# Kernel tuning notes

Hardware: AMD Instinct MI355X
Metric: run time of the kernel (lower is better)

Reference implementation:

```python
import jax, jax.numpy as jnp
import numpy as np

H, W, D = 160, 160, 16
VOXEL_SIZE = 0.4
VOL_MIN = np.array([-32.0, -32.0, -1.0], dtype=np.float32)
SCALE_MULTIPLIER = 3.0
N_GAUSS = 8192
CHUNK = 64


def setup_inputs() -> dict:
    key = jax.random.key(0)
    k1, k2, k3, k4, k5 = jax.random.split(key, 5)
    vol_min = jnp.asarray(VOL_MIN)
    vol_ext = jnp.array([64.0, 64.0, 6.4], dtype=jnp.float32)
    means3d = jax.random.uniform(k1, (N_GAUSS, 3), jnp.float32) * vol_ext + vol_min
    opacities = jax.random.uniform(k2, (N_GAUSS, 1), jnp.float32)
    # per-axis std devs: 0.2..0.8 m so 3-sigma footprint spans a handful of voxels
    scales = 0.2 + 0.6 * jax.random.uniform(k3, (N_GAUSS, 3), jnp.float32)
    rotations = jax.random.normal(k4, (N_GAUSS, 4), jnp.float32)
    features = jax.random.normal(k5, (N_GAUSS, 32), jnp.float32)
    return {"means3d": means3d, "opacities": opacities, "scales": scales,
            "rotations": rotations, "features": features}


def quat_to_rotmat(q):
    # q: [N,4] wxyz, normalized
    w, x, y, z = q[:, 0], q[:, 1], q[:, 2], q[:, 3]
    R = jnp.stack([
        jnp.stack([1 - 2 * (y * y + z * z), 2 * (x * y - w * z), 2 * (x * z + w * y)], -1),
        jnp.stack([2 * (x * y + w * z), 1 - 2 * (x * x + z * z), 2 * (y * z - w * x)], -1),
        jnp.stack([2 * (x * z - w * y), 2 * (y * z + w * x), 1 - 2 * (x * x + y * y)], -1),
    ], axis=-2)  # [N,3,3]
    return R


def _grid_coords():
    ii, jj, kk = jnp.meshgrid(jnp.arange(H), jnp.arange(W), jnp.arange(D), indexing="ij")
    idx = jnp.stack([ii, jj, kk], axis=-1).astype(jnp.float32)
    return (idx + 0.5) * VOXEL_SIZE + jnp.asarray(VOL_MIN)  # [H,W,D,3] voxel centers


def reference(means3d, opacities, scales, rotations, features):
    x = _grid_coords().reshape(-1, 3)  # [V,3]
    q = rotations / jnp.linalg.norm(rotations, axis=-1, keepdims=True)
    R = quat_to_rotmat(q)
    # covariance = R diag(s^2) R^T
    cov = jnp.einsum("nij,nj,nkj->nik", R, scales * scales, R)
    cov_inv = jnp.linalg.inv(cov)
    sigma = jnp.sqrt(jnp.diagonal(cov, axis1=1, axis2=2))  # [N,3]
    opac = opacities[:, 0]  # [N]
    n = means3d.shape[0]
    nchunks = n // CHUNK

    def chunked(a):
        return a.reshape(nchunks, CHUNK, *a.shape[1:])

    def step(acc, c):
        mu, op, sg, ci, ft = c
        diff = x[:, None, :] - mu[None, :, :]  # [V,CHUNK,3]
        maha = jnp.einsum("vci,cij,vcj->vc", diff, ci, diff)
        # local aggregation cutoff: within scale_multiplier * sigma box around mean
        mask = jnp.all(jnp.abs(diff) <= SCALE_MULTIPLIER * sg[None, :, :], axis=-1)
        w = op[None, :] * jnp.exp(-0.5 * maha) * mask  # [V,CHUNK]
        return acc + w @ ft, None

    acc0 = jnp.zeros((x.shape[0], features.shape[-1]), jnp.float32)
    xs = (chunked(means3d), chunked(opac), chunked(sigma), chunked(cov_inv), chunked(features))
    acc, _ = jax.lax.scan(step, acc0, xs)
    return acc.reshape(H, W, D, features.shape[-1])
```

## Files before the change

### kernel.cpp

```cpp
#include <hip/hip_runtime.h>

#define HH 160
#define WW 160
#define DD 16
#define NG 8192
#define VOXEL 0.4f

#define TTX 20
#define TTY 20
#define TTZ 4
#define NTILES (TTX * TTY * TTZ)
#define CAP 128


__global__ __launch_bounds__(64) void gv_precompute_bin(
    const float* __restrict__ means, const float* __restrict__ opac,
    const float* __restrict__ scales, const float* __restrict__ rots,
    int* __restrict__ tileCnt, float4* __restrict__ tilePack) {
  int g = blockIdx.x * 64 + threadIdx.x;
  if (g >= NG) return;
  float qw = rots[g * 4 + 0], qx = rots[g * 4 + 1];
  float qy = rots[g * 4 + 2], qz = rots[g * 4 + 3];
  float inv = rsqrtf(qw * qw + qx * qx + qy * qy + qz * qz);
  qw *= inv; qx *= inv; qy *= inv; qz *= inv;
  float R[3][3];
  R[0][0] = 1.f - 2.f * (qy * qy + qz * qz);
  R[0][1] = 2.f * (qx * qy - qw * qz);
  R[0][2] = 2.f * (qx * qz + qw * qy);
  R[1][0] = 2.f * (qx * qy + qw * qz);
  R[1][1] = 1.f - 2.f * (qx * qx + qz * qz);
  R[1][2] = 2.f * (qy * qz - qw * qx);
  R[2][0] = 2.f * (qx * qz - qw * qy);
  R[2][1] = 2.f * (qy * qz + qw * qx);
  R[2][2] = 1.f - 2.f * (qx * qx + qy * qy);
  float sx = scales[g * 3 + 0], sy = scales[g * 3 + 1], sz = scales[g * 3 + 2];
  float s2[3] = {sx * sx, sy * sy, sz * sz};
  float is2[3] = {1.f / s2[0], 1.f / s2[1], 1.f / s2[2]};
  float cov00 = 0.f, cov11 = 0.f, cov22 = 0.f;
  float ci00 = 0.f, ci01 = 0.f, ci02 = 0.f, ci11 = 0.f, ci12 = 0.f, ci22 = 0.f;
#pragma unroll
  for (int c = 0; c < 3; c++) {
    cov00 += R[0][c] * R[0][c] * s2[c];
    cov11 += R[1][c] * R[1][c] * s2[c];
    cov22 += R[2][c] * R[2][c] * s2[c];
    ci00 += R[0][c] * R[0][c] * is2[c];
    ci01 += R[0][c] * R[1][c] * is2[c];
    ci02 += R[0][c] * R[2][c] * is2[c];
    ci11 += R[1][c] * R[1][c] * is2[c];
    ci12 += R[1][c] * R[2][c] * is2[c];
    ci22 += R[2][c] * R[2][c] * is2[c];
  }
  float mx = means[g * 3 + 0], my = means[g * 3 + 1], mz = means[g * 3 + 2];
  float bx = 3.f * sqrtf(cov00), by = 3.f * sqrtf(cov11), bz = 3.f * sqrtf(cov22);

  const float eps = 1e-4f;
  int i0 = (int)ceilf((mx - bx + 32.f) * 2.5f - 0.5f - eps);
  int i1 = (int)floorf((mx + bx + 32.f) * 2.5f - 0.5f + eps);
  int j0 = (int)ceilf((my - by + 32.f) * 2.5f - 0.5f - eps);
  int j1 = (int)floorf((my + by + 32.f) * 2.5f - 0.5f + eps);
  int k0 = (int)ceilf((mz - bz + 1.f) * 2.5f - 0.5f - eps);
  int k1 = (int)floorf((mz + bz + 1.f) * 2.5f - 0.5f + eps);
  i0 = max(i0, 0); i1 = min(i1, HH - 1);
  j0 = max(j0, 0); j1 = min(j1, WW - 1);
  k0 = max(k0, 0); k1 = min(k1, DD - 1);
  if (i0 > i1 || j0 > j1 || k0 > k1) return;

  float4 p0 = make_float4(mx, my, mz, opac[g]);
  float4 p1 = make_float4(bx, by, bz, __int_as_float(g));
  float4 p2 = make_float4(ci00, ci01, ci02, ci11);
  float4 p3 = make_float4(ci12, ci22, 0.f, 0.f);

  int ti0 = i0 >> 3, ti1 = i1 >> 3;
  int tj0 = j0 >> 3, tj1 = j1 >> 3;
  int tk0 = k0 >> 2, tk1 = k1 >> 2;
  for (int ti = ti0; ti <= ti1; ti++)
    for (int tj = tj0; tj <= tj1; tj++)
      for (int tk = tk0; tk <= tk1; tk++) {
        int t = (ti * TTY + tj) * TTZ + tk;
        int pos = atomicAdd(&tileCnt[t], 1);
        if (pos < CAP) {
          float4* __restrict__ d = tilePack + ((size_t)t * CAP + pos) * 4;
          d[0] = p0;  d[1] = p1;  d[2] = p2;  d[3] = p3;
        }
      }
}

__global__ __launch_bounds__(256) void gv_voxelize(
    const float4* __restrict__ feats, const int* __restrict__ tileCnt,
    const float4* __restrict__ tilePack, float4* __restrict__ out) {
  __shared__ float4 s_pack[CAP * 4];

  int tid = threadIdx.x;
  int dk = tid & 3, dj = (tid >> 2) & 7, di = tid >> 5;
  int tk = blockIdx.x, tj = blockIdx.y, ti = blockIdx.z;
  int i = ti * 8 + di, j = tj * 8 + dj, k = tk * 4 + dk;

  float px = (i + 0.5f) * VOXEL - 32.f;
  float py = (j + 0.5f) * VOXEL - 32.f;
  float pz = (k + 0.5f) * VOXEL - 1.f;

  int t = (ti * TTY + tj) * TTZ + tk;
  int cnt = tileCnt[t];
  cnt = min(cnt, CAP);

  {
    const float4* __restrict__ src = tilePack + (size_t)t * CAP * 4;
    int tot = cnt * 4;
    for (int m = tid; m < tot; m += 256) s_pack[m] = src[m];
  }
  __syncthreads();

  float4 acc[8];
#pragma unroll
  for (int f = 0; f < 8; f++) acc[f] = make_float4(0.f, 0.f, 0.f, 0.f);

  int n = 0;
  for (; n + 2 <= cnt; n += 2) {
    float4 a0 = s_pack[n * 4 + 0], b0 = s_pack[n * 4 + 1];
    float4 a1 = s_pack[n * 4 + 4], b1 = s_pack[n * 4 + 5];

    int g0 = __builtin_amdgcn_readfirstlane(__float_as_int(b0.w));
    int g1 = __builtin_amdgcn_readfirstlane(__float_as_int(b1.w));
    const float4* __restrict__ fp0 = feats + (size_t)g0 * 8;
    const float4* __restrict__ fp1 = feats + (size_t)g1 * 8;
    float4 F0[8], F1[8];
#pragma unroll
    for (int f = 0; f < 8; f++) F0[f] = fp0[f];
#pragma unroll
    for (int f = 0; f < 8; f++) F1[f] = fp1[f];

    float dx0 = px - a0.x, dy0 = py - a0.y, dz0 = pz - a0.z;
    float dx1 = px - a1.x, dy1 = py - a1.y, dz1 = pz - a1.z;
    bool in0 = (fabsf(dx0) <= b0.x) & (fabsf(dy0) <= b0.y) & (fabsf(dz0) <= b0.z);
    bool in1 = (fabsf(dx1) <= b1.x) & (fabsf(dy1) <= b1.y) & (fabsf(dz1) <= b1.z);

    if (__any(in0)) {
      float4 c0 = s_pack[n * 4 + 2], d0 = s_pack[n * 4 + 3];
      float maha = c0.x * dx0 * dx0 + c0.w * dy0 * dy0 + d0.y * dz0 * dz0 +
                   2.f * (c0.y * dx0 * dy0 + c0.z * dx0 * dz0 + d0.x * dy0 * dz0);
      float wgt = in0 ? a0.w * __expf(-0.5f * maha) : 0.f;
#pragma unroll
      for (int f = 0; f < 8; f++) {
        acc[f].x += wgt * F0[f].x;
        acc[f].y += wgt * F0[f].y;
        acc[f].z += wgt * F0[f].z;
        acc[f].w += wgt * F0[f].w;
      }
    }
    if (__any(in1)) {
      float4 c1 = s_pack[n * 4 + 6], d1 = s_pack[n * 4 + 7];
      float maha = c1.x * dx1 * dx1 + c1.w * dy1 * dy1 + d1.y * dz1 * dz1 +
                   2.f * (c1.y * dx1 * dy1 + c1.z * dx1 * dz1 + d1.x * dy1 * dz1);
      float wgt = in1 ? a1.w * __expf(-0.5f * maha) : 0.f;
#pragma unroll
      for (int f = 0; f < 8; f++) {
        acc[f].x += wgt * F1[f].x;
        acc[f].y += wgt * F1[f].y;
        acc[f].z += wgt * F1[f].z;
        acc[f].w += wgt * F1[f].w;
      }
    }
  }
  if (n < cnt) {
    float4 pa = s_pack[n * 4 + 0], pb = s_pack[n * 4 + 1];
    int gg = __builtin_amdgcn_readfirstlane(__float_as_int(pb.w));
    const float4* __restrict__ fp = feats + (size_t)gg * 8;
    float dx = px - pa.x, dy = py - pa.y, dz = pz - pa.z;
    bool in = (fabsf(dx) <= pb.x) & (fabsf(dy) <= pb.y) & (fabsf(dz) <= pb.z);
    if (__any(in)) {
      float4 pc = s_pack[n * 4 + 2], pd = s_pack[n * 4 + 3];
      float maha = pc.x * dx * dx + pc.w * dy * dy + pd.y * dz * dz +
                   2.f * (pc.y * dx * dy + pc.z * dx * dz + pd.x * dy * dz);
      float wgt = in ? pa.w * __expf(-0.5f * maha) : 0.f;
#pragma unroll
      for (int f = 0; f < 8; f++) {
        float4 fv = fp[f];
        acc[f].x += wgt * fv.x;
        acc[f].y += wgt * fv.y;
        acc[f].z += wgt * fv.z;
        acc[f].w += wgt * fv.w;
      }
    }
  }

  size_t v = ((size_t)i * WW + j) * DD + k;
  float4* o = out + v * 8;
#pragma unroll
  for (int f = 0; f < 8; f++) o[f] = acc[f];
}

extern "C" void kernel_launch(void* const* d_in, const int* in_sizes, int n_in,
                              void* d_out, int out_size, void* d_ws, size_t ws_size,
                              hipStream_t stream) {
  const float* means  = (const float*)d_in[0];
  const float* opac   = (const float*)d_in[1];
  const float* scales = (const float*)d_in[2];
  const float* rots   = (const float*)d_in[3];
  const float4* feats = (const float4*)d_in[4];

  char* ws = (char*)d_ws;
  int* tileCnt     = (int*)ws;
  float4* tilePack = (float4*)(ws + 64 * 1024);

  hipMemsetAsync(tileCnt, 0, NTILES * sizeof(int), stream);
  gv_precompute_bin<<<128, 64, 0, stream>>>(means, opac, scales, rots,
                                            tileCnt, tilePack);
  dim3 grid(TTZ, TTY, TTX);
  gv_voxelize<<<grid, 256, 0, stream>>>(feats, tileCnt, tilePack,
                                        (float4*)d_out);
}
```

Measured before the change: 121.9 us.

## Compute two voxels per thread to reuse gaussian loads and shared terms

Each thread now handles two voxels at j and j+4, so the block shrinks to 128 threads and every lane reuses one set of loaded gaussian features and shared mahalanobis terms (x/z parts) across both voxels. This cuts the per-voxel cost of feature loads, LDS reads, wave-level any-votes and loop overhead. The trade-off is twice the accumulator registers, which may lower occupancy, and fewer waves per block. The any-vote now covers a union of two voxel rows, so some waves may run gaussians that only one of their voxels needs.

```diff
diff --git a/kernel.cpp b/kernel.cpp
--- a/kernel.cpp
+++ b/kernel.cpp
@@ -85,18 +85,20 @@
       }
 }
 
-__global__ __launch_bounds__(256) void gv_voxelize(
+__global__ __launch_bounds__(128) void gv_voxelize(
     const float4* __restrict__ feats, const int* __restrict__ tileCnt,
     const float4* __restrict__ tilePack, float4* __restrict__ out) {
   __shared__ float4 s_pack[CAP * 4];
 
   int tid = threadIdx.x;
-  int dk = tid & 3, dj = (tid >> 2) & 7, di = tid >> 5;
+  int wid = tid >> 6, l = tid & 63;
+  int dk = l & 3, dj = (l >> 2) & 3, di = wid * 4 + (l >> 4);
   int tk = blockIdx.x, tj = blockIdx.y, ti = blockIdx.z;
-  int i = ti * 8 + di, j = tj * 8 + dj, k = tk * 4 + dk;
+  int i = ti * 8 + di, jA = tj * 8 + dj, jB = jA + 4, k = tk * 4 + dk;
 
   float px = (i + 0.5f) * VOXEL - 32.f;
-  float py = (j + 0.5f) * VOXEL - 32.f;
+  float pyA = (jA + 0.5f) * VOXEL - 32.f;
+  float pyB = (jB + 0.5f) * VOXEL - 32.f;
   float pz = (k + 0.5f) * VOXEL - 1.f;
 
   int t = (ti * TTY + tj) * TTZ + tk;
@@ -106,13 +108,41 @@
   {
     const float4* __restrict__ src = tilePack + (size_t)t * CAP * 4;
     int tot = cnt * 4;
-    for (int m = tid; m < tot; m += 256) s_pack[m] = src[m];
+    for (int m = tid; m < tot; m += 128) s_pack[m] = src[m];
   }
   __syncthreads();
 
-  float4 acc[8];
-#pragma unroll
-  for (int f = 0; f < 8; f++) acc[f] = make_float4(0.f, 0.f, 0.f, 0.f);
+  float4 accA[8], accB[8];
+#pragma unroll
+  for (int f = 0; f < 8; f++) {
+    accA[f] = make_float4(0.f, 0.f, 0.f, 0.f);
+    accB[f] = make_float4(0.f, 0.f, 0.f, 0.f);
+  }
+
+#define GAUSS_BODY(aa, bb, cidx, didx, FF)                                    \
+  do {                                                                        \
+    float dx = px - aa.x, dz = pz - aa.z;                                     \
+    float dyA = pyA - aa.y, dyB = pyB - aa.y;                                 \
+    bool okx = (fabsf(dx) <= bb.x) & (fabsf(dz) <= bb.z);                     \
+    bool inA = okx & (fabsf(dyA) <= bb.y);                                    \
+    bool inB = okx & (fabsf(dyB) <= bb.y);                                    \
+    if (__any(inA | inB)) {                                                   \
+      float4 cc = s_pack[cidx], dd = s_pack[didx];                            \
+      float base = cc.x * dx * dx + dd.y * dz * dz + 2.f * cc.z * dx * dz;    \
+      float u = 2.f * (cc.y * dx + dd.x * dz);                                \
+      float mA = base + dyA * (cc.w * dyA + u);                               \
+      float mB = base + dyB * (cc.w * dyB + u);                               \
+      float wA = inA ? aa.w * __expf(-0.5f * mA) : 0.f;                       \
+      float wB = inB ? aa.w * __expf(-0.5f * mB) : 0.f;                       \
+      _Pragma("unroll")                                                       \
+      for (int f = 0; f < 8; f++) {                                           \
+        accA[f].x += wA * FF[f].x; accA[f].y += wA * FF[f].y;                 \
+        accA[f].z += wA * FF[f].z; accA[f].w += wA * FF[f].w;                 \
+        accB[f].x += wB * FF[f].x; accB[f].y += wB * FF[f].y;                 \
+        accB[f].z += wB * FF[f].z; accB[f].w += wB * FF[f].w;                 \
+      }                                                                       \
+    }                                                                         \
+  } while (0)
 
   int n = 0;
   for (; n + 2 <= cnt; n += 2) {
@@ -129,64 +159,28 @@
 #pragma unroll
     for (int f = 0; f < 8; f++) F1[f] = fp1[f];
 
-    float dx0 = px - a0.x, dy0 = py - a0.y, dz0 = pz - a0.z;
-    float dx1 = px - a1.x, dy1 = py - a1.y, dz1 = pz - a1.z;
-    bool in0 = (fabsf(dx0) <= b0.x) & (fabsf(dy0) <= b0.y) & (fabsf(dz0) <= b0.z);
-    bool in1 = (fabsf(dx1) <= b1.x) & (fabsf(dy1) <= b1.y) & (fabsf(dz1) <= b1.z);
-
-    if (__any(in0)) {
-      float4 c0 = s_pack[n * 4 + 2], d0 = s_pack[n * 4 + 3];
-      float maha = c0.x * dx0 * dx0 + c0.w * dy0 * dy0 + d0.y * dz0 * dz0 +
-                   2.f * (c0.y * dx0 * dy0 + c0.z * dx0 * dz0 + d0.x * dy0 * dz0);
-      float wgt = in0 ? a0.w * __expf(-0.5f * maha) : 0.f;
-#pragma unroll
-      for (int f = 0; f < 8; f++) {
-        acc[f].x += wgt * F0[f].x;
-        acc[f].y += wgt * F0[f].y;
-        acc[f].z += wgt * F0[f].z;
-        acc[f].w += wgt * F0[f].w;
-      }
-    }
-    if (__any(in1)) {
-      float4 c1 = s_pack[n * 4 + 6], d1 = s_pack[n * 4 + 7];
-      float maha = c1.x * dx1 * dx1 + c1.w * dy1 * dy1 + d1.y * dz1 * dz1 +
-                   2.f * (c1.y * dx1 * dy1 + c1.z * dx1 * dz1 + d1.x * dy1 * dz1);
-      float wgt = in1 ? a1.w * __expf(-0.5f * maha) : 0.f;
-#pragma unroll
-      for (int f = 0; f < 8; f++) {
-        acc[f].x += wgt * F1[f].x;
-        acc[f].y += wgt * F1[f].y;
-        acc[f].z += wgt * F1[f].z;
-        acc[f].w += wgt * F1[f].w;
-      }
-    }
+    GAUSS_BODY(a0, b0, n * 4 + 2, n * 4 + 3, F0);
+    GAUSS_BODY(a1, b1, n * 4 + 6, n * 4 + 7, F1);
   }
   if (n < cnt) {
     float4 pa = s_pack[n * 4 + 0], pb = s_pack[n * 4 + 1];
     int gg = __builtin_amdgcn_readfirstlane(__float_as_int(pb.w));
     const float4* __restrict__ fp = feats + (size_t)gg * 8;
-    float dx = px - pa.x, dy = py - pa.y, dz = pz - pa.z;
-    bool in = (fabsf(dx) <= pb.x) & (fabsf(dy) <= pb.y) & (fabsf(dz) <= pb.z);
-    if (__any(in)) {
-      float4 pc = s_pack[n * 4 + 2], pd = s_pack[n * 4 + 3];
-      float maha = pc.x * dx * dx + pc.w * dy * dy + pd.y * dz * dz +
-                   2.f * (pc.y * dx * dy + pc.z * dx * dz + pd.x * dy * dz);
-      float wgt = in ? pa.w * __expf(-0.5f * maha) : 0.f;
-#pragma unroll
-      for (int f = 0; f < 8; f++) {
-        float4 fv = fp[f];
-        acc[f].x += wgt * fv.x;
-        acc[f].y += wgt * fv.y;
-        acc[f].z += wgt * fv.z;
-        acc[f].w += wgt * fv.w;
-      }
-    }
-  }
-
-  size_t v = ((size_t)i * WW + j) * DD + k;
-  float4* o = out + v * 8;
-#pragma unroll
-  for (int f = 0; f < 8; f++) o[f] = acc[f];
+    float4 FT[8];
+#pragma unroll
+    for (int f = 0; f < 8; f++) FT[f] = fp[f];
+    GAUSS_BODY(pa, pb, n * 4 + 2, n * 4 + 3, FT);
+  }
+#undef GAUSS_BODY
+
+  size_t vA = ((size_t)i * WW + jA) * DD + k;
+  size_t vB = ((size_t)i * WW + jB) * DD + k;
+  float4* oA = out + vA * 8;
+  float4* oB = out + vB * 8;
+#pragma unroll
+  for (int f = 0; f < 8; f++) oA[f] = accA[f];
+#pragma unroll
+  for (int f = 0; f < 8; f++) oB[f] = accB[f];
 }
 
 extern "C" void kernel_launch(void* const* d_in, const int* in_sizes, int n_in,
@@ -206,6 +200,6 @@
   gv_precompute_bin<<<128, 64, 0, stream>>>(means, opac, scales, rots,
                                             tileCnt, tilePack);
   dim3 grid(TTZ, TTY, TTX);
-  gv_voxelize<<<grid, 256, 0, stream>>>(feats, tileCnt, tilePack,
+  gv_voxelize<<<grid, 128, 0, stream>>>(feats, tileCnt, tilePack,
                                         (float4*)d_out);
 }
```

Measured after the change: 127.6 us. 4.7% more time.

## Split tile gaussian list across two wave halves and reduce via LDS

Applied to the files above, without the earlier changes.

The voxelize block grows from 256 to 512 threads. Two groups of waves cover the same voxels and take alternating pairs of gaussians from the tile list, then combine their partial sums through shared memory in two stages before the store. Each wave also now covers a compact 4x4x4 voxel sub-cube instead of a 2x8x4 slab, which should make the wave-level `__any` box cull skip more often. This doubles the parallelism per tile and shortens the serial loop over gaussians. The cost is extra LDS traffic, three more barriers, and duplicated feature loads across the two halves.

```diff
diff --git a/kernel.cpp b/kernel.cpp
--- a/kernel.cpp
+++ b/kernel.cpp
@@ -85,13 +85,19 @@
       }
 }
 
-__global__ __launch_bounds__(256) void gv_voxelize(
+__global__ __launch_bounds__(512) void gv_voxelize(
     const float4* __restrict__ feats, const int* __restrict__ tileCnt,
     const float4* __restrict__ tilePack, float4* __restrict__ out) {
   __shared__ float4 s_pack[CAP * 4];
+  __shared__ float4 s_red[2][64][9];
 
   int tid = threadIdx.x;
-  int dk = tid & 3, dj = (tid >> 2) & 7, di = tid >> 5;
+  int wid = tid >> 6, l = tid & 63;
+  int sub = wid >> 1;
+  int h = wid & 1;
+  int dk = l & 3;
+  int dj = (sub & 1) * 4 + ((l >> 2) & 3);
+  int di = (sub >> 1) * 4 + (l >> 4);
   int tk = blockIdx.x, tj = blockIdx.y, ti = blockIdx.z;
   int i = ti * 8 + di, j = tj * 8 + dj, k = tk * 4 + dk;
 
@@ -106,7 +112,7 @@
   {
     const float4* __restrict__ src = tilePack + (size_t)t * CAP * 4;
     int tot = cnt * 4;
-    for (int m = tid; m < tot; m += 256) s_pack[m] = src[m];
+    for (int m = tid; m < tot; m += 512) s_pack[m] = src[m];
   }
   __syncthreads();
 
@@ -114,8 +120,8 @@
 #pragma unroll
   for (int f = 0; f < 8; f++) acc[f] = make_float4(0.f, 0.f, 0.f, 0.f);
 
-  int n = 0;
-  for (; n + 2 <= cnt; n += 2) {
+  int n = 2 * h;
+  for (; n + 2 <= cnt; n += 4) {
     float4 a0 = s_pack[n * 4 + 0], b0 = s_pack[n * 4 + 1];
     float4 a1 = s_pack[n * 4 + 4], b1 = s_pack[n * 4 + 5];
 
@@ -185,8 +191,34 @@
 
   size_t v = ((size_t)i * WW + j) * DD + k;
   float4* o = out + v * 8;
-#pragma unroll
-  for (int f = 0; f < 8; f++) o[f] = acc[f];
+
+  if (h && sub < 2) {
+#pragma unroll
+    for (int f = 0; f < 8; f++) s_red[sub][l][f] = acc[f];
+  }
+  __syncthreads();
+  if (!h && sub < 2) {
+#pragma unroll
+    for (int f = 0; f < 8; f++) {
+      float4 r = s_red[sub][l][f];
+      o[f] = make_float4(acc[f].x + r.x, acc[f].y + r.y,
+                         acc[f].z + r.z, acc[f].w + r.w);
+    }
+  }
+  __syncthreads();
+  if (h && sub >= 2) {
+#pragma unroll
+    for (int f = 0; f < 8; f++) s_red[sub - 2][l][f] = acc[f];
+  }
+  __syncthreads();
+  if (!h && sub >= 2) {
+#pragma unroll
+    for (int f = 0; f < 8; f++) {
+      float4 r = s_red[sub - 2][l][f];
+      o[f] = make_float4(acc[f].x + r.x, acc[f].y + r.y,
+                         acc[f].z + r.z, acc[f].w + r.w);
+    }
+  }
 }
 
 extern "C" void kernel_launch(void* const* d_in, const int* in_sizes, int n_in,
@@ -206,6 +238,6 @@
   gv_precompute_bin<<<128, 64, 0, stream>>>(means, opac, scales, rots,
                                             tileCnt, tilePack);
   dim3 grid(TTZ, TTY, TTX);
-  gv_voxelize<<<grid, 256, 0, stream>>>(feats, tileCnt, tilePack,
+  gv_voxelize<<<grid, 512, 0, stream>>>(feats, tileCnt, tilePack,
                                         (float4*)d_out);
 }
```

After: 122.6 us. Within noise of the previous version (+0.6%).
